# Kernel optimization log

Measured on AMD Instinct MI355X. Metric: run time of the kernel, lower is better.

Reference implementation:

```python
import jax, jax.numpy as jnp
import numpy as np

EPS_SUM = 1e-5   # clamp on soft-assignment mass
EPS_NORM = 1e-12  # F.normalize eps


def setup_inputs() -> dict:
    key = jax.random.key(0)
    k1, k2, k3 = jax.random.split(key, 3)
    bs, ch, h, w = 64, 256, 56, 56
    num_parts = 3
    featmaps = jax.random.normal(k1, (bs, ch, h, w), dtype=jnp.float32)
    # kaiming-normal-like init for centers, clamped positive as in init_parameters
    part_centers = jnp.clip(
        jax.random.normal(k2, (num_parts, ch), dtype=jnp.float32) * np.sqrt(2.0 / ch),
        1e-5, None)
    part_smooth_factors = jax.random.normal(k3, (num_parts,), dtype=jnp.float32) * 0.1
    return {"featmaps": featmaps, "part_centers": part_centers,
            "part_smooth_factors": part_smooth_factors}


def reference(featmaps, part_centers, part_smooth_factors):
    bs, ch, h, w = featmaps.shape
    k = part_centers.shape[0]
    x = featmaps.reshape(bs, ch, h * w)                      # [bs, ch, n]

    # distance terms
    cx = jnp.einsum('kc,bcn->bkn', part_centers, x)          # [bs, k, n]
    x_sq = jnp.sum(x * x, axis=1, keepdims=True)             # [bs, 1, n]
    c_sq = jnp.sum(part_centers * part_centers, axis=1)      # [k]

    beta = jax.nn.sigmoid(part_smooth_factors)               # [k]
    logits = jnp.minimum(2.0 * cx - x_sq - c_sq[None, :, None], 0.0) / beta[None, :, None]
    assign = jax.nn.softmax(logits, axis=1)                  # softmax over parts, [bs, k, n]

    # weighted pooling
    qx = jnp.einsum('bkn,bcn->bkc', assign, x)               # [bs, k, ch]
    sum_ass = jnp.maximum(jnp.sum(assign, axis=2, keepdims=True), EPS_SUM)  # [bs, k, 1]
    qx_ = qx / sum_ass

    sigma = jnp.sqrt(beta / 2.0)                             # [k]
    out = (qx_ - part_centers[None]) / sigma[None, :, None]  # [bs, k, ch]
    norm = jnp.maximum(jnp.linalg.norm(out, axis=2, keepdims=True), EPS_NORM)
    outputs = (out / norm).transpose(0, 2, 1)                # [bs, ch, k]

    return outputs, assign.reshape(bs, k, h, w)
```

## Files before the change

kernel.cpp:

```cpp
#include <hip/hip_runtime.h>
#include <math.h>

#define BS   64
#define CH   256
#define NPIX 3136
#define NK   3
#define TILE 512
#define TPB  256
#define TILES_PER_IMG 7

#define QX_ELEMS (BS*NK*CH)
#define SA_ELEMS (BS*NK)

__global__ __launch_bounds__(TPB)
void pgn_assign(const float* __restrict__ x,
                const float* __restrict__ centers,
                const float* __restrict__ psf,
                float* __restrict__ assign_out,
                float* __restrict__ qx,
                float* __restrict__ sa)
{
    __shared__ float4 ctr4[CH];
    __shared__ float  a_sh[NK][TILE];
    __shared__ float  csq_sh[NK];
    __shared__ float  sa_sh[NK];

    const int tid = threadIdx.x;
    const int bid = blockIdx.x;
    const int b   = bid / TILES_PER_IMG;
    const int t   = bid % TILES_PER_IMG;
    const int n0  = t * TILE + tid * 2;
    const bool valid = (n0 < NPIX);

    {
        const float c0 = centers[0*CH + tid];
        const float c1 = centers[1*CH + tid];
        const float c2 = centers[2*CH + tid];
        ctr4[tid] = make_float4(c0, c1, c2, 0.f);
        if (tid < NK) sa_sh[tid] = 0.f;
    }
    __syncthreads();
    if (tid < NK) {
        const float* cf = (const float*)ctr4;
        float s = 0.f;
        #pragma unroll 8
        for (int c = 0; c < CH; ++c) { const float u = cf[4*c + tid]; s = fmaf(u, u, s); }
        csq_sh[tid] = s;
    }
    __syncthreads();

    const float rb0 = 1.f + __expf(-psf[0]);
    const float rb1 = 1.f + __expf(-psf[1]);
    const float rb2 = 1.f + __expf(-psf[2]);
    const float cs0 = csq_sh[0], cs1 = csq_sh[1], cs2 = csq_sh[2];

    float a00=0.f,a01=0.f,a10=0.f,a11=0.f,a20=0.f,a21=0.f;
    if (valid) {
        const float* xb = x + (size_t)b * CH * NPIX + n0;
        float cx00=0.f,cx01=0.f,cx10=0.f,cx11=0.f,cx20=0.f,cx21=0.f,xs0=0.f,xs1=0.f;
        #pragma unroll 4
        for (int c = 0; c < CH; ++c) {
            const float2 xv = *(const float2*)(xb + (size_t)c * NPIX);
            const float4 cc = ctr4[c];
            cx00 = fmaf(cc.x, xv.x, cx00); cx01 = fmaf(cc.x, xv.y, cx01);
            cx10 = fmaf(cc.y, xv.x, cx10); cx11 = fmaf(cc.y, xv.y, cx11);
            cx20 = fmaf(cc.z, xv.x, cx20); cx21 = fmaf(cc.z, xv.y, cx21);
            xs0  = fmaf(xv.x, xv.x, xs0);  xs1  = fmaf(xv.y, xv.y, xs1);
        }
        {
            const float l0 = fminf(2.f*cx00 - xs0 - cs0, 0.f) * rb0;
            const float l1 = fminf(2.f*cx10 - xs0 - cs1, 0.f) * rb1;
            const float l2 = fminf(2.f*cx20 - xs0 - cs2, 0.f) * rb2;
            const float m  = fmaxf(l0, fmaxf(l1, l2));
            const float e0 = __expf(l0 - m), e1 = __expf(l1 - m), e2 = __expf(l2 - m);
            const float inv = 1.f / (e0 + e1 + e2);
            a00 = e0*inv; a10 = e1*inv; a20 = e2*inv;
        }
        {
            const float l0 = fminf(2.f*cx01 - xs1 - cs0, 0.f) * rb0;
            const float l1 = fminf(2.f*cx11 - xs1 - cs1, 0.f) * rb1;
            const float l2 = fminf(2.f*cx21 - xs1 - cs2, 0.f) * rb2;
            const float m  = fmaxf(l0, fmaxf(l1, l2));
            const float e0 = __expf(l0 - m), e1 = __expf(l1 - m), e2 = __expf(l2 - m);
            const float inv = 1.f / (e0 + e1 + e2);
            a01 = e0*inv; a11 = e1*inv; a21 = e2*inv;
        }
        float* ao = assign_out + (size_t)b * NK * NPIX + n0;
        *(float2*)(ao)            = make_float2(a00, a01);
        *(float2*)(ao + NPIX)     = make_float2(a10, a11);
        *(float2*)(ao + 2*NPIX)   = make_float2(a20, a21);
    }
    a_sh[0][tid*2] = a00; a_sh[0][tid*2+1] = a01;
    a_sh[1][tid*2] = a10; a_sh[1][tid*2+1] = a11;
    a_sh[2][tid*2] = a20; a_sh[2][tid*2+1] = a21;
    const float s0 = a00 + a01, s1 = a10 + a11, s2 = a20 + a21;
    if (valid) {
        atomicAdd(&sa_sh[0], s0);
        atomicAdd(&sa_sh[1], s1);
        atomicAdd(&sa_sh[2], s2);
    }
    __syncthreads();

    const int nbase  = t * TILE;
    const int nvalid = (NPIX - nbase < TILE) ? (NPIX - nbase) : TILE;
    const float* xr  = x + ((size_t)b * CH + tid) * NPIX + nbase;
    float q0 = 0.f, q1 = 0.f, q2 = 0.f;
    #pragma unroll 8
    for (int p = 0; p < nvalid; p += 4) {
        const float4 xv = *(const float4*)(xr + p);
        const float4 A0 = *(const float4*)&a_sh[0][p];
        const float4 A1 = *(const float4*)&a_sh[1][p];
        const float4 A2 = *(const float4*)&a_sh[2][p];
        q0 = fmaf(A0.x, xv.x, fmaf(A0.y, xv.y, fmaf(A0.z, xv.z, fmaf(A0.w, xv.w, q0))));
        q1 = fmaf(A1.x, xv.x, fmaf(A1.y, xv.y, fmaf(A1.z, xv.z, fmaf(A1.w, xv.w, q1))));
        q2 = fmaf(A2.x, xv.x, fmaf(A2.y, xv.y, fmaf(A2.z, xv.z, fmaf(A2.w, xv.w, q2))));
    }
    float* qb = qx + (size_t)b * NK * CH + tid;
    atomicAdd(qb,          q0);
    atomicAdd(qb + CH,     q1);
    atomicAdd(qb + 2*CH,   q2);

    if (tid < NK) atomicAdd(&sa[b*NK + tid], sa_sh[tid]);
}

__global__ __launch_bounds__(TPB)
void pgn_final(const float* __restrict__ qx,
               const float* __restrict__ sa,
               const float* __restrict__ centers,
               const float* __restrict__ psf,
               float* __restrict__ out)
{
    const int b = blockIdx.x;
    const int c = threadIdx.x;
    const int wave = c >> 6, lane = c & 63;
    __shared__ float red[4][NK];
    __shared__ float nrm[NK];

    float v[NK];
    float ss[NK];
    #pragma unroll
    for (int k = 0; k < NK; ++k) {
        const float beta = 1.f / (1.f + __expf(-psf[k]));
        const float sig  = sqrtf(0.5f * beta);
        const float s    = fmaxf(sa[b*NK + k], 1e-5f);
        const float q    = qx[((size_t)b*NK + k)*CH + c] / s;
        v[k]  = (q - centers[k*CH + c]) / sig;
        ss[k] = v[k] * v[k];
    }
    #pragma unroll
    for (int m = 32; m; m >>= 1) {
        ss[0] += __shfl_xor(ss[0], m, 64);
        ss[1] += __shfl_xor(ss[1], m, 64);
        ss[2] += __shfl_xor(ss[2], m, 64);
    }
    if (lane == 0) { red[wave][0] = ss[0]; red[wave][1] = ss[1]; red[wave][2] = ss[2]; }
    __syncthreads();
    if (c < NK) {
        const float tot = red[0][c] + red[1][c] + red[2][c] + red[3][c];
        nrm[c] = fmaxf(sqrtf(tot), 1e-12f);
    }
    __syncthreads();
    float* o = out + ((size_t)b*CH + c)*NK;
    #pragma unroll
    for (int k = 0; k < NK; ++k) o[k] = v[k] / nrm[k];
}

extern "C" void kernel_launch(void* const* d_in, const int* in_sizes, int n_in,
                              void* d_out, int out_size, void* d_ws, size_t ws_size,
                              hipStream_t stream)
{
    const float* feat    = (const float*)d_in[0];
    const float* centers = (const float*)d_in[1];
    const float* psf     = (const float*)d_in[2];

    float* out        = (float*)d_out;
    float* assign_out = out + (size_t)BS*CH*NK;

    float* qx = (float*)d_ws;
    float* sa = qx + QX_ELEMS;

    hipMemsetAsync(d_ws, 0, (QX_ELEMS + SA_ELEMS) * sizeof(float), stream);

    pgn_assign<<<dim3(BS * TILES_PER_IMG), dim3(TPB), 0, stream>>>(
        feat, centers, psf, assign_out, qx, sa);

    pgn_final<<<dim3(BS), dim3(TPB), 0, stream>>>(qx, sa, centers, psf, out);
}
```

Before: 326.2 us.

## Split fused assign/pool kernel into separate high-occupancy assign and pooling kernels

Replaces the single fused kernel, which computed soft assignments and then pooled per 512-pixel tile with global atomics on qx, with four kernels. A tiny setup kernel precomputes interleaved centers, squared norms and inverse betas. The assign kernel handles one pixel per thread over more blocks and reduces assignment mass with wave shuffles. A separate pool kernel computes qx per group of 8 channels without atomics. This raises parallelism and removes qx atomics and the qx memset, at the cost of reading the feature map a second time in a separate pass, plus extra launches.

```diff
diff --git a/kernel.cpp b/kernel.cpp
--- a/kernel.cpp
+++ b/kernel.cpp
@@ -5,127 +5,156 @@
 #define CH   256
 #define NPIX 3136
 #define NK   3
-#define TILE 512
-#define TPB  256
-#define TILES_PER_IMG 7
-
-#define QX_ELEMS (BS*NK*CH)
-#define SA_ELEMS (BS*NK)
-
-__global__ __launch_bounds__(TPB)
+
+#define WS_CSQ   0
+#define WS_RB    4
+#define WS_CTR4  8
+#define WS_SA    (8 + CH*4)
+#define WS_QX    (WS_SA + BS*NK)
+
+__global__ __launch_bounds__(64)
+void pgn_setup(const float* __restrict__ centers, const float* __restrict__ psf,
+               float* __restrict__ ws)
+{
+    const int lane = threadIdx.x;
+    float4* ctr4 = (float4*)(ws + WS_CTR4);
+    #pragma unroll
+    for (int j = 0; j < 4; ++j) {
+        const int c = lane * 4 + j;
+        ctr4[c] = make_float4(centers[c], centers[CH + c], centers[2*CH + c], 0.f);
+    }
+    #pragma unroll
+    for (int k = 0; k < NK; ++k) {
+        float s = 0.f;
+        #pragma unroll
+        for (int j = 0; j < 4; ++j) {
+            const float u = centers[k*CH + lane*4 + j];
+            s = fmaf(u, u, s);
+        }
+        #pragma unroll
+        for (int m = 32; m; m >>= 1) s += __shfl_xor(s, m, 64);
+        if (lane == 0) ws[WS_CSQ + k] = s;
+    }
+    if (lane < NK) ws[WS_RB + lane] = 1.f + __expf(-psf[lane]);
+}
+
+#define TILE1 256
+#define NT1   13
+
+__global__ __launch_bounds__(256)
 void pgn_assign(const float* __restrict__ x,
-                const float* __restrict__ centers,
-                const float* __restrict__ psf,
+                const float* __restrict__ ws,
                 float* __restrict__ assign_out,
-                float* __restrict__ qx,
                 float* __restrict__ sa)
 {
-    __shared__ float4 ctr4[CH];
-    __shared__ float  a_sh[NK][TILE];
-    __shared__ float  csq_sh[NK];
-    __shared__ float  sa_sh[NK];
-
+    __shared__ float4 ctr[CH];
     const int tid = threadIdx.x;
-    const int bid = blockIdx.x;
-    const int b   = bid / TILES_PER_IMG;
-    const int t   = bid % TILES_PER_IMG;
-    const int n0  = t * TILE + tid * 2;
-    const bool valid = (n0 < NPIX);
-
-    {
-        const float c0 = centers[0*CH + tid];
-        const float c1 = centers[1*CH + tid];
-        const float c2 = centers[2*CH + tid];
-        ctr4[tid] = make_float4(c0, c1, c2, 0.f);
-        if (tid < NK) sa_sh[tid] = 0.f;
-    }
-    __syncthreads();
-    if (tid < NK) {
-        const float* cf = (const float*)ctr4;
-        float s = 0.f;
+    const int b   = blockIdx.x / NT1;
+    const int t   = blockIdx.x % NT1;
+    const int n   = t * TILE1 + tid;
+
+    ctr[tid] = ((const float4*)(ws + WS_CTR4))[tid];
+    __syncthreads();
+
+    const float cs0 = ws[WS_CSQ+0], cs1 = ws[WS_CSQ+1], cs2 = ws[WS_CSQ+2];
+    const float rb0 = ws[WS_RB+0],  rb1 = ws[WS_RB+1],  rb2 = ws[WS_RB+2];
+
+    float a0 = 0.f, a1 = 0.f, a2 = 0.f;
+    if (n < NPIX) {
+        const float* xb = x + (size_t)b * CH * NPIX + n;
+        float c0 = 0.f, c1 = 0.f, c2 = 0.f, xs = 0.f;
         #pragma unroll 8
-        for (int c = 0; c < CH; ++c) { const float u = cf[4*c + tid]; s = fmaf(u, u, s); }
-        csq_sh[tid] = s;
-    }
-    __syncthreads();
-
-    const float rb0 = 1.f + __expf(-psf[0]);
-    const float rb1 = 1.f + __expf(-psf[1]);
-    const float rb2 = 1.f + __expf(-psf[2]);
-    const float cs0 = csq_sh[0], cs1 = csq_sh[1], cs2 = csq_sh[2];
-
-    float a00=0.f,a01=0.f,a10=0.f,a11=0.f,a20=0.f,a21=0.f;
-    if (valid) {
-        const float* xb = x + (size_t)b * CH * NPIX + n0;
-        float cx00=0.f,cx01=0.f,cx10=0.f,cx11=0.f,cx20=0.f,cx21=0.f,xs0=0.f,xs1=0.f;
-        #pragma unroll 4
         for (int c = 0; c < CH; ++c) {
-            const float2 xv = *(const float2*)(xb + (size_t)c * NPIX);
-            const float4 cc = ctr4[c];
-            cx00 = fmaf(cc.x, xv.x, cx00); cx01 = fmaf(cc.x, xv.y, cx01);
-            cx10 = fmaf(cc.y, xv.x, cx10); cx11 = fmaf(cc.y, xv.y, cx11);
-            cx20 = fmaf(cc.z, xv.x, cx20); cx21 = fmaf(cc.z, xv.y, cx21);
-            xs0  = fmaf(xv.x, xv.x, xs0);  xs1  = fmaf(xv.y, xv.y, xs1);
-        }
-        {
-            const float l0 = fminf(2.f*cx00 - xs0 - cs0, 0.f) * rb0;
-            const float l1 = fminf(2.f*cx10 - xs0 - cs1, 0.f) * rb1;
-            const float l2 = fminf(2.f*cx20 - xs0 - cs2, 0.f) * rb2;
-            const float m  = fmaxf(l0, fmaxf(l1, l2));
-            const float e0 = __expf(l0 - m), e1 = __expf(l1 - m), e2 = __expf(l2 - m);
-            const float inv = 1.f / (e0 + e1 + e2);
-            a00 = e0*inv; a10 = e1*inv; a20 = e2*inv;
-        }
-        {
-            const float l0 = fminf(2.f*cx01 - xs1 - cs0, 0.f) * rb0;
-            const float l1 = fminf(2.f*cx11 - xs1 - cs1, 0.f) * rb1;
-            const float l2 = fminf(2.f*cx21 - xs1 - cs2, 0.f) * rb2;
-            const float m  = fmaxf(l0, fmaxf(l1, l2));
-            const float e0 = __expf(l0 - m), e1 = __expf(l1 - m), e2 = __expf(l2 - m);
-            const float inv = 1.f / (e0 + e1 + e2);
-            a01 = e0*inv; a11 = e1*inv; a21 = e2*inv;
-        }
-        float* ao = assign_out + (size_t)b * NK * NPIX + n0;
-        *(float2*)(ao)            = make_float2(a00, a01);
-        *(float2*)(ao + NPIX)     = make_float2(a10, a11);
-        *(float2*)(ao + 2*NPIX)   = make_float2(a20, a21);
-    }
-    a_sh[0][tid*2] = a00; a_sh[0][tid*2+1] = a01;
-    a_sh[1][tid*2] = a10; a_sh[1][tid*2+1] = a11;
-    a_sh[2][tid*2] = a20; a_sh[2][tid*2+1] = a21;
-    const float s0 = a00 + a01, s1 = a10 + a11, s2 = a20 + a21;
-    if (valid) {
-        atomicAdd(&sa_sh[0], s0);
-        atomicAdd(&sa_sh[1], s1);
-        atomicAdd(&sa_sh[2], s2);
-    }
-    __syncthreads();
-
-    const int nbase  = t * TILE;
-    const int nvalid = (NPIX - nbase < TILE) ? (NPIX - nbase) : TILE;
-    const float* xr  = x + ((size_t)b * CH + tid) * NPIX + nbase;
-    float q0 = 0.f, q1 = 0.f, q2 = 0.f;
-    #pragma unroll 8
-    for (int p = 0; p < nvalid; p += 4) {
-        const float4 xv = *(const float4*)(xr + p);
-        const float4 A0 = *(const float4*)&a_sh[0][p];
-        const float4 A1 = *(const float4*)&a_sh[1][p];
-        const float4 A2 = *(const float4*)&a_sh[2][p];
-        q0 = fmaf(A0.x, xv.x, fmaf(A0.y, xv.y, fmaf(A0.z, xv.z, fmaf(A0.w, xv.w, q0))));
-        q1 = fmaf(A1.x, xv.x, fmaf(A1.y, xv.y, fmaf(A1.z, xv.z, fmaf(A1.w, xv.w, q1))));
-        q2 = fmaf(A2.x, xv.x, fmaf(A2.y, xv.y, fmaf(A2.z, xv.z, fmaf(A2.w, xv.w, q2))));
-    }
-    float* qb = qx + (size_t)b * NK * CH + tid;
-    atomicAdd(qb,          q0);
-    atomicAdd(qb + CH,     q1);
-    atomicAdd(qb + 2*CH,   q2);
-
-    if (tid < NK) atomicAdd(&sa[b*NK + tid], sa_sh[tid]);
-}
-
-__global__ __launch_bounds__(TPB)
-void pgn_final(const float* __restrict__ qx,
-               const float* __restrict__ sa,
+            const float  xv = xb[(size_t)c * NPIX];
+            const float4 cc = ctr[c];
+            c0 = fmaf(cc.x, xv, c0);
+            c1 = fmaf(cc.y, xv, c1);
+            c2 = fmaf(cc.z, xv, c2);
+            xs = fmaf(xv, xv, xs);
+        }
+        const float l0 = fminf(2.f*c0 - xs - cs0, 0.f) * rb0;
+        const float l1 = fminf(2.f*c1 - xs - cs1, 0.f) * rb1;
+        const float l2 = fminf(2.f*c2 - xs - cs2, 0.f) * rb2;
+        const float m  = fmaxf(l0, fmaxf(l1, l2));
+        const float e0 = __expf(l0 - m), e1 = __expf(l1 - m), e2 = __expf(l2 - m);
+        const float inv = 1.f / (e0 + e1 + e2);
+        a0 = e0 * inv; a1 = e1 * inv; a2 = e2 * inv;
+
+        float* ao = assign_out + (size_t)b * NK * NPIX + n;
+        ao[0]        = a0;
+        ao[NPIX]     = a1;
+        ao[2*NPIX]   = a2;
+    }
+
+    float s0 = a0, s1 = a1, s2 = a2;
+    #pragma unroll
+    for (int m = 32; m; m >>= 1) {
+        s0 += __shfl_xor(s0, m, 64);
+        s1 += __shfl_xor(s1, m, 64);
+        s2 += __shfl_xor(s2, m, 64);
+    }
+    if ((tid & 63) == 0) {
+        atomicAdd(&sa[b*NK + 0], s0);
+        atomicAdd(&sa[b*NK + 1], s1);
+        atomicAdd(&sa[b*NK + 2], s2);
+    }
+}
+
+#define CPB 8
+#define NCB (CH/CPB)
+
+__global__ __launch_bounds__(256)
+void pgn_pool(const float* __restrict__ x,
+              const float* __restrict__ assign,
+              float* __restrict__ qx)
+{
+    const int tid = threadIdx.x;
+    const int b   = blockIdx.x / NCB;
+    const int c0  = (blockIdx.x % NCB) * CPB;
+
+    const float* ab = assign + (size_t)b * NK * NPIX;
+    const float* xb = x + ((size_t)b * CH + c0) * NPIX;
+
+    float q[CPB][NK];
+    #pragma unroll
+    for (int j = 0; j < CPB; ++j)
+        #pragma unroll
+        for (int k = 0; k < NK; ++k) q[j][k] = 0.f;
+
+    for (int p = tid * 4; p + 3 < NPIX; p += 256 * 4) {
+        const float4 A0 = *(const float4*)(ab + p);
+        const float4 A1 = *(const float4*)(ab + NPIX + p);
+        const float4 A2 = *(const float4*)(ab + 2*NPIX + p);
+        #pragma unroll
+        for (int j = 0; j < CPB; ++j) {
+            const float4 xv = *(const float4*)(xb + (size_t)j * NPIX + p);
+            q[j][0] = fmaf(A0.x, xv.x, fmaf(A0.y, xv.y, fmaf(A0.z, xv.z, fmaf(A0.w, xv.w, q[j][0]))));
+            q[j][1] = fmaf(A1.x, xv.x, fmaf(A1.y, xv.y, fmaf(A1.z, xv.z, fmaf(A1.w, xv.w, q[j][1]))));
+            q[j][2] = fmaf(A2.x, xv.x, fmaf(A2.y, xv.y, fmaf(A2.z, xv.z, fmaf(A2.w, xv.w, q[j][2]))));
+        }
+    }
+
+    __shared__ float part[4][CPB*NK];
+    const int wave = tid >> 6, lane = tid & 63;
+    #pragma unroll
+    for (int j = 0; j < CPB; ++j)
+        #pragma unroll
+        for (int k = 0; k < NK; ++k) {
+            float v = q[j][k];
+            #pragma unroll
+            for (int m = 32; m; m >>= 1) v += __shfl_xor(v, m, 64);
+            if (lane == 0) part[wave][j*NK + k] = v;
+        }
+    __syncthreads();
+    if (tid < CPB*NK) {
+        const float tot = part[0][tid] + part[1][tid] + part[2][tid] + part[3][tid];
+        const int j = tid / NK, k = tid % NK;
+        qx[((size_t)b*NK + k)*CH + c0 + j] = tot;
+    }
+}
+
+__global__ __launch_bounds__(256)
+void pgn_final(const float* __restrict__ ws,
                const float* __restrict__ centers,
                const float* __restrict__ psf,
                float* __restrict__ out)
@@ -136,8 +165,10 @@
     __shared__ float red[4][NK];
     __shared__ float nrm[NK];
 
-    float v[NK];
-    float ss[NK];
+    const float* qx = ws + WS_QX;
+    const float* sa = ws + WS_SA;
+
+    float v[NK], ss[NK];
     #pragma unroll
     for (int k = 0; k < NK; ++k) {
         const float beta = 1.f / (1.f + __expf(-psf[k]));
@@ -176,13 +207,14 @@
     float* out        = (float*)d_out;
     float* assign_out = out + (size_t)BS*CH*NK;
 
-    float* qx = (float*)d_ws;
-    float* sa = qx + QX_ELEMS;
-
-    hipMemsetAsync(d_ws, 0, (QX_ELEMS + SA_ELEMS) * sizeof(float), stream);
-
-    pgn_assign<<<dim3(BS * TILES_PER_IMG), dim3(TPB), 0, stream>>>(
-        feat, centers, psf, assign_out, qx, sa);
-
-    pgn_final<<<dim3(BS), dim3(TPB), 0, stream>>>(qx, sa, centers, psf, out);
-}
+    float* ws = (float*)d_ws;
+    float* sa = ws + WS_SA;
+    float* qx = ws + WS_QX;
+
+    hipMemsetAsync(sa, 0, BS*NK*sizeof(float), stream);
+
+    pgn_setup<<<dim3(1), dim3(64), 0, stream>>>(centers, psf, ws);
+    pgn_assign<<<dim3(BS*NT1), dim3(256), 0, stream>>>(feat, ws, assign_out, sa);
+    pgn_pool<<<dim3(BS*NCB), dim3(256), 0, stream>>>(feat, assign_out, qx);
+    pgn_final<<<dim3(BS), dim3(256), 0, stream>>>(ws, centers, psf, out);
+}
```

New measurement: 335.6 us. +2.9%, slower.
